# Performance work log

Measured on AMD Instinct MI355X. Metric: run time of the kernel, lower is better.

The kernel has to match this reference:

```python
import jax, jax.numpy as jnp
import numpy as np

T, B, V, E, HID, K = 1024, 128, 65536, 128, 256, 64
H = HID // 2  # per-direction LSTM hidden


def setup_inputs() -> dict:
    key = jax.random.key(0)
    ks = jax.random.split(key, 18)
    s = 0.05
    f32 = jnp.float32
    return {
        "kmers": jax.random.randint(ks[0], (T, B), 0, V),
        "tags": jax.random.randint(ks[1], (B,), 0, K),
        "emb": jax.random.normal(ks[2], (V, E), f32) * s,
        "w_ih_f": jax.random.normal(ks[3], (4 * H, E), f32) * s,
        "w_hh_f": jax.random.normal(ks[4], (4 * H, H), f32) * s,
        "b_ih_f": jax.random.normal(ks[5], (4 * H,), f32) * s,
        "b_hh_f": jax.random.normal(ks[6], (4 * H,), f32) * s,
        "w_ih_b": jax.random.normal(ks[7], (4 * H, E), f32) * s,
        "w_hh_b": jax.random.normal(ks[8], (4 * H, H), f32) * s,
        "b_ih_b": jax.random.normal(ks[9], (4 * H,), f32) * s,
        "b_hh_b": jax.random.normal(ks[10], (4 * H,), f32) * s,
        "w_proj": jax.random.normal(ks[11], (K, HID), f32) * s,
        "b_proj": jax.random.normal(ks[12], (K,), f32) * s,
        "start_trans": jax.random.uniform(ks[13], (K,), f32, -0.1, 0.1),
        "end_trans": jax.random.uniform(ks[14], (K,), f32, -0.1, 0.1),
        "trans": jax.random.uniform(ks[15], (K, K), f32, -0.1, 0.1),
    }


def _lstm_dir(x, w_ih, w_hh, b_ih, b_hh):
    # x: [T, B, E] -> hidden states [T, B, H]; PyTorch gate order i,f,g,o
    b = b_ih + b_hh
    xg = jnp.einsum('tbe,ge->tbg', x, w_ih) + b  # precompute input gates
    Bd = x.shape[1]
    Hd = w_hh.shape[1]
    def step(carry, g_in):
        h, c = carry
        g = g_in + h @ w_hh.T
        i, f, gg, o = jnp.split(g, 4, axis=-1)
        c = jax.nn.sigmoid(f) * c + jax.nn.sigmoid(i) * jnp.tanh(gg)
        h = jax.nn.sigmoid(o) * jnp.tanh(c)
        return (h, c), h
    init = (jnp.zeros((Bd, Hd), x.dtype), jnp.zeros((Bd, Hd), x.dtype))
    _, hs = jax.lax.scan(step, init, xg)
    return hs


def reference(kmers, tags, emb, w_ih_f, w_hh_f, b_ih_f, b_hh_f,
              w_ih_b, w_hh_b, b_ih_b, b_hh_b, w_proj, b_proj,
              start_trans, end_trans, trans):
    x = emb[kmers]  # [T, B, E]
    h_f = _lstm_dir(x, w_ih_f, w_hh_f, b_ih_f, b_hh_f)
    h_b = _lstm_dir(x[::-1], w_ih_b, w_hh_b, b_ih_b, b_hh_b)[::-1]
    out = jnp.concatenate([h_f, h_b], axis=-1)  # [T, B, HID]
    emissions = jnp.einsum('tbh,kh->tbk', out, w_proj) + b_proj  # [T, B, K]

    # tags repeated along time (original: tags.repeat(sent_size, 1))
    tags_seq = jnp.broadcast_to(tags[None, :], (emissions.shape[0], tags.shape[0]))

    # CRF numerator: score of given tag sequence (full mask)
    em_sel = jnp.take_along_axis(emissions, tags_seq[:, :, None], axis=2)[..., 0]  # [T, B]
    numerator = (start_trans[tags_seq[0]] + em_sel.sum(0)
                 + trans[tags_seq[:-1], tags_seq[1:]].sum(0)
                 + end_trans[tags_seq[-1]])  # [B]

    # CRF denominator: forward algorithm (log partition)
    def fwd_step(score, em_t):
        # score: [B, K] -> logsumexp over previous tag
        nxt = jax.nn.logsumexp(score[:, :, None] + trans[None, :, :] + em_t[:, None, :], axis=1)
        return nxt, None
    init = start_trans[None, :] + emissions[0]  # [B, K]
    final, _ = jax.lax.scan(fwd_step, init, emissions[1:])
    denominator = jax.nn.logsumexp(final + end_trans[None, :], axis=1)  # [B]

    # torchcrf default reduction='sum'; module returns negated llh
    return (denominator - numerator).sum()
```

## Files before the change

### kernel.cpp

```cpp
#include <hip/hip_runtime.h>
#include <hip/hip_bf16.h>

typedef _Float16 half8_t __attribute__((ext_vector_type(8)));
typedef _Float16 half4_t __attribute__((ext_vector_type(4)));
typedef _Float16 half2_t __attribute__((ext_vector_type(2)));
typedef float float4_t __attribute__((ext_vector_type(4)));
typedef unsigned int uint2_t __attribute__((ext_vector_type(2)));

#define TT 1024
#define BB 128
#define EE 128
#define HH 128
#define NTAG 64
#define ASTR 144

__device__ __forceinline__ float fast_exp(float x) {
  return __builtin_amdgcn_exp2f(x * 1.44269504088896f);
}
__device__ __forceinline__ void lds_barrier() {
  asm volatile("s_waitcnt lgkmcnt(0)\n\ts_barrier" ::: "memory");
}
__device__ __forceinline__ void lds_fence() {
  asm volatile("s_waitcnt lgkmcnt(0)" ::: "memory");
}
__device__ __forceinline__ half2_t cvt_pk(float a, float b) {
  return __builtin_bit_cast(half2_t, __builtin_amdgcn_cvt_pkrtz(a, b));
}
__device__ __forceinline__ half2_t h2bc(float v) {
  _Float16 h = (_Float16)v;
  half2_t r; r[0] = h; r[1] = h;
  return r;
}
__device__ __forceinline__ half8_t h8bc(float v) {
  _Float16 h = (_Float16)v;
  half8_t r;
#pragma unroll
  for (int i = 0; i < 8; ++i) r[i] = h;
  return r;
}
__device__ __forceinline__ float quad_max4(float v) {
  unsigned a = __builtin_bit_cast(unsigned, v);
  uint2_t r = __builtin_amdgcn_permlane32_swap(a, a, false, false);
  float m = fmaxf(__builtin_bit_cast(float, r[0]), __builtin_bit_cast(float, r[1]));
  unsigned b = __builtin_bit_cast(unsigned, m);
  uint2_t s = __builtin_amdgcn_permlane16_swap(b, b, false, false);
  return fmaxf(__builtin_bit_cast(float, s[0]), __builtin_bit_cast(float, s[1]));
}
__device__ __forceinline__ half2_t tanh6(half2_t x) {
  half2_t y = __builtin_elementwise_min(__builtin_elementwise_max(x, h2bc(-1.6f)), h2bc(1.6f));
  half2_t u = y * y;
  half2_t p = u * h2bc(0.04667f) + h2bc(-0.28507f);
  p = u * p + h2bc(1.0f);
  return y * p;
}
__device__ __forceinline__ half2_t sig6(half2_t x) {
  half2_t y = __builtin_elementwise_min(__builtin_elementwise_max(x, h2bc(-3.2f)), h2bc(3.2f));
  half2_t u = y * y;
  half2_t q = u * h2bc(0.00072921875f) + h2bc(-0.017816875f);
  q = u * q + h2bc(0.25f);
  return y * q + h2bc(0.5f);
}

__global__ __launch_bounds__(256) void initembed_kernel(const int* __restrict__ kmers,
                                                        const float* __restrict__ emb,
                                                        half4_t* __restrict__ x,
                                                        float4_t* __restrict__ state,
                                                        float* __restrict__ out) {
  if (blockIdx.x < 48) {
    if (blockIdx.x == 0 && threadIdx.x == 0) out[0] = 0.f;
    state[blockIdx.x * 256 + threadIdx.x] = (float4_t){0.f, 0.f, 0.f, 0.f};
    return;
  }
  const int g = (blockIdx.x - 48) * 256 + threadIdx.x;
  const int row = g >> 5, seg = g & 31;
  const int km = kmers[row];
  const float4_t v = ((const float4_t*)(emb + (size_t)km * EE))[seg];
  half4_t o;
  o[0] = (_Float16)v[0]; o[1] = (_Float16)v[1];
  o[2] = (_Float16)v[2]; o[3] = (_Float16)v[3];
  x[(size_t)row * 32 + seg] = o;
}

__device__ __forceinline__ void xg_body(
    int wg, int tid, const _Float16* __restrict__ x,
    const float* __restrict__ w_ih_f, const float* __restrict__ b_ih_f, const float* __restrict__ b_hh_f,
    const float* __restrict__ w_ih_b, const float* __restrict__ b_ih_b, const float* __restrict__ b_hh_b,
    _Float16* __restrict__ xgbuf, int s, int Tseg) {
  const int nt = Tseg >> 4;
  const int dir = wg / (8 * nt);
  const int rem = wg - dir * 8 * nt;
  const int chunk = rem / nt;
  const int tb = rem - chunk * nt;
  const int wave = tid >> 6, lane = tid & 63;
  const int n16 = lane & 15, quad = lane >> 4;

  const float* wih = dir ? w_ih_b : w_ih_f;
  const float* bih = dir ? b_ih_b : b_ih_f;
  const float* bhh = dir ? b_hh_b : b_hh_f;

  half8_t wf[4][4];
#pragma unroll
  for (int g = 0; g < 4; ++g) {
    const int row = g * HH + wave * 16 + n16;
#pragma unroll
    for (int kf = 0; kf < 4; ++kf) {
      const float* src = wih + row * EE + kf * 32 + quad * 8;
#pragma unroll
      for (int i = 0; i < 8; ++i) wf[g][kf][i] = (_Float16)src[i];
    }
  }
  float4_t bias4[4];
#pragma unroll
  for (int g = 0; g < 4; ++g) {
    const int row = g * HH + wave * 16 + quad * 4;
    const float4_t bi = *(const float4_t*)(bih + row);
    const float4_t bh = *(const float4_t*)(bhh + row);
    bias4[g] = bi + bh;
  }

  const int l0 = tb * 16;
  half8_t xb[4];
  {
    const int te = dir ? (TT - 1 - (s * Tseg + l0)) : (s * Tseg + l0);
#pragma unroll
    for (int kf = 0; kf < 4; ++kf)
      xb[kf] = *(const half8_t*)(x + ((size_t)te * BB + chunk * 16 + n16) * EE + kf * 32 + quad * 8);
  }
  for (int u = 0; u < 16; ++u) {
    const int l = l0 + u;
    half8_t xn[4] = {};
    if (u < 15) {
      const int tn = dir ? (TT - 1 - (s * Tseg + l + 1)) : (s * Tseg + l + 1);
#pragma unroll
      for (int kf = 0; kf < 4; ++kf)
        xn[kf] = *(const half8_t*)(x + ((size_t)tn * BB + chunk * 16 + n16) * EE + kf * 32 + quad * 8);
    }
    float4_t acc[4];
#pragma unroll
    for (int g = 0; g < 4; ++g) acc[g] = bias4[g];
#pragma unroll
    for (int kf = 0; kf < 4; ++kf)
#pragma unroll
      for (int g = 0; g < 4; ++g)
        acc[g] = __builtin_amdgcn_mfma_f32_16x16x32_f16(wf[g][kf], xb[kf], acc[g], 0, 0, 0);
    half8_t ho0, ho1;
#pragma unroll
    for (int r = 0; r < 4; ++r) {
      ho0[r] = (_Float16)acc[0][r];
      ho0[4 + r] = (_Float16)acc[1][r];
      ho1[r] = (_Float16)acc[2][r];
      ho1[4 + r] = (_Float16)acc[3][r];
    }
    _Float16* ob = xgbuf + (size_t)dir * Tseg * 65536 + (size_t)l * 65536 + chunk * 8192 +
                   wave * 1024 + lane * 16;
    *(half8_t*)ob = ho0;
    *(half8_t*)(ob + 8) = ho1;
#pragma unroll
    for (int kf = 0; kf < 4; ++kf) xb[kf] = xn[kf];
  }
}

__global__ __launch_bounds__(512) void xg_kernel(
    const _Float16* __restrict__ x,
    const float* __restrict__ w_ih_f, const float* __restrict__ b_ih_f, const float* __restrict__ b_hh_f,
    const float* __restrict__ w_ih_b, const float* __restrict__ b_ih_b, const float* __restrict__ b_hh_b,
    _Float16* __restrict__ xgbuf, int s, int Tseg) {
  xg_body(blockIdx.x, threadIdx.x, x, w_ih_f, b_ih_f, b_hh_f, w_ih_b, b_ih_b, b_hh_b, xgbuf, s,
          Tseg);
}

__global__ __launch_bounds__(512, 2) void lstm_xg_kernel(
    const _Float16* __restrict__ xgrd, _Float16* __restrict__ xgwr,
    const _Float16* __restrict__ x,
    const float* __restrict__ w_hh_f, const float* __restrict__ w_hh_b,
    const float* __restrict__ w_ih_f, const float* __restrict__ b_ih_f, const float* __restrict__ b_hh_f,
    const float* __restrict__ w_ih_b, const float* __restrict__ b_ih_b, const float* __restrict__ b_hh_b,
    _Float16* __restrict__ h_cat, _Float16* __restrict__ h_state, float* __restrict__ c_state,
    int s, int sx, int Tseg) {
  __shared__ _Float16 A[2][16 * ASTR];
  if (blockIdx.x >= 16) {
    xg_body(blockIdx.x - 16, threadIdx.x, x, w_ih_f, b_ih_f, b_hh_f, w_ih_b, b_ih_b, b_hh_b,
            xgwr, sx, Tseg);
    return;
  }
  const int wg = blockIdx.x;
  const int dir = wg >> 3, chunk = wg & 7;
  const int b0 = chunk * 16;
  const float* w_hh = dir ? w_hh_b : w_hh_f;
  const int tid = threadIdx.x;
  const int wave = tid >> 6, lane = tid & 63;
  const int n16 = lane & 15, quad = lane >> 4;

  half8_t wf[4][4];
#pragma unroll
  for (int g = 0; g < 4; ++g) {
    const int row = g * HH + wave * 16 + n16;
#pragma unroll
    for (int kf = 0; kf < 4; ++kf) {
      const float* src = w_hh + row * HH + kf * 32 + quad * 8;
#pragma unroll
      for (int i = 0; i < 8; ++i) wf[g][kf][i] = (_Float16)src[i];
    }
  }
  const int sidx = ((wg * 8 + wave) * 64 + lane) * 4;
  half4_t h4 = *(const half4_t*)(h_state + sidx);
  float4_t c4 = *(const float4_t*)(c_state + sidx);
  half2_t c2[2];
  c2[0] = cvt_pk(c4[0], c4[1]);
  c2[1] = cvt_pk(c4[2], c4[3]);
  *(half4_t*)(&A[0][n16 * ASTR + wave * 16 + quad * 4]) = h4;

  const _Float16* xgw =
      xgrd + (size_t)dir * Tseg * 65536 + chunk * 8192 + wave * 1024 + (size_t)lane * 16;
  half4_t hlast = h4;
  const float4_t z4 = {0.f, 0.f, 0.f, 0.f};
  const int te0 = dir ? (TT - 1 - s * Tseg) : (s * Tseg);
  _Float16* gp_run =
      h_cat + ((size_t)te0 * BB + b0 + n16) * 256 + dir * HH + wave * 16 + quad * 4;
  const ptrdiff_t dstep = dir ? -(ptrdiff_t)32768 : (ptrdiff_t)32768;

  half8_t pf0[4], pf1[4];
#pragma unroll
  for (int j = 0; j < 4; ++j) {
    const _Float16* p = xgw + (size_t)j * 65536;
    pf0[j] = *(const half8_t*)p;
    pf1[j] = *(const half8_t*)(p + 8);
  }

#define LSTM_STEP(AB, AN, X0, X1)                                                          \
  {                                                                                        \
    const _Float16* Abp = &AB[0];                                                          \
    _Float16* Anp = &AN[0];                                                                \
    half8_t hb0 = *(const half8_t*)(Abp + n16 * ASTR + 0 * 32 + quad * 8);                 \
    half8_t hb1 = *(const half8_t*)(Abp + n16 * ASTR + 1 * 32 + quad * 8);                 \
    half8_t hb2 = *(const half8_t*)(Abp + n16 * ASTR + 2 * 32 + quad * 8);                 \
    half8_t hb3 = *(const half8_t*)(Abp + n16 * ASTR + 3 * 32 + quad * 8);                 \
    float4_t acc[4];                                                                       \
    _Pragma("unroll") for (int g = 0; g < 4; ++g) {                                        \
      acc[g] = __builtin_amdgcn_mfma_f32_16x16x32_f16(wf[g][0], hb0, z4, 0, 0, 0);         \
    }                                                                                      \
    _Pragma("unroll") for (int g = 0; g < 4; ++g) {                                        \
      acc[g] = __builtin_amdgcn_mfma_f32_16x16x32_f16(wf[g][1], hb1, acc[g], 0, 0, 0);     \
    }                                                                                      \
    _Pragma("unroll") for (int g = 0; g < 4; ++g) {                                        \
      acc[g] = __builtin_amdgcn_mfma_f32_16x16x32_f16(wf[g][2], hb2, acc[g], 0, 0, 0);     \
    }                                                                                      \
    _Pragma("unroll") for (int g = 0; g < 4; ++g) {                                        \
      acc[g] = __builtin_amdgcn_mfma_f32_16x16x32_f16(wf[g][3], hb3, acc[g], 0, 0, 0);     \
    }                                                                                      \
    const half2_t* x0p = (const half2_t*)&X0;                                              \
    const half2_t* x1p = (const half2_t*)&X1;                                              \
    half4_t hstore;                                                                        \
    _Pragma("unroll") for (int p = 0; p < 2; ++p) {                                        \
      const half2_t i_ = sig6(cvt_pk(acc[0][2 * p], acc[0][2 * p + 1]) + x0p[p]);          \
      const half2_t f_ = sig6(cvt_pk(acc[1][2 * p], acc[1][2 * p + 1]) + x0p[2 + p]);      \
      const half2_t g_ = tanh6(cvt_pk(acc[2][2 * p], acc[2][2 * p + 1]) + x1p[p]);         \
      const half2_t o_ = sig6(cvt_pk(acc[3][2 * p], acc[3][2 * p + 1]) + x1p[2 + p]);      \
      c2[p] = f_ * c2[p] + i_ * g_;                                                        \
      const half2_t hh = o_ * tanh6(c2[p]);                                                \
      hstore[2 * p] = hh[0];                                                               \
      hstore[2 * p + 1] = hh[1];                                                           \
    }                                                                                      \
    *(half4_t*)(Anp + n16 * ASTR + wave * 16 + quad * 4) = hstore;                         \
    *(half4_t*)gp_run = hstore;                                                            \
    hlast = hstore;                                                                        \
  }

  for (int il = 0; il < Tseg - 4; il += 4) {
#pragma unroll
    for (int j = 0; j < 4; ++j) {
      lds_barrier();
      if (j & 1) {
        LSTM_STEP(A[1], A[0], pf0[j], pf1[j]);
      } else {
        LSTM_STEP(A[0], A[1], pf0[j], pf1[j]);
      }
      const _Float16* p = xgw + (size_t)(il + j + 4) * 65536;
      pf0[j] = *(const half8_t*)p;
      pf1[j] = *(const half8_t*)(p + 8);
      gp_run += dstep;
    }
  }
#pragma unroll
  for (int j = 0; j < 4; ++j) {
    lds_barrier();
    if (j & 1) {
      LSTM_STEP(A[1], A[0], pf0[j], pf1[j]);
    } else {
      LSTM_STEP(A[0], A[1], pf0[j], pf1[j]);
    }
    gp_run += dstep;
  }
#undef LSTM_STEP

  *(half4_t*)(h_state + sidx) = hlast;
  c4[0] = (float)c2[0][0]; c4[1] = (float)c2[0][1];
  c4[2] = (float)c2[1][0]; c4[3] = (float)c2[1][1];
  *(float4_t*)(c_state + sidx) = c4;
}

__global__ __launch_bounds__(256) void emis_kernel(const _Float16* __restrict__ h_cat,
                                                   const float* __restrict__ w_proj,
                                                   const float* __restrict__ b_proj,
                                                   float* __restrict__ em,
                                                   _Float16* __restrict__ expem) {
  const int tid = threadIdx.x;
  const int wave = tid >> 6, lane = tid & 63;
  const int n16 = lane & 15, quad = lane >> 4;
  const size_t row0 = (size_t)blockIdx.x * 64 + wave * 16;

  half8_t bf[4][8];
#pragma unroll
  for (int nt = 0; nt < 4; ++nt) {
    const float* wp = w_proj + (nt * 16 + n16) * 256;
#pragma unroll
    for (int kf = 0; kf < 8; ++kf) {
      const int kb = kf * 32 + quad * 8;
#pragma unroll
      for (int i = 0; i < 8; ++i) bf[nt][kf][i] = (_Float16)wp[kb + i];
    }
  }
  float4_t acc[4];
#pragma unroll
  for (int nt = 0; nt < 4; ++nt) {
    const float bv = b_proj[nt * 16 + n16];
    acc[nt] = (float4_t){bv, bv, bv, bv};
  }
#pragma unroll
  for (int kf = 0; kf < 8; ++kf) {
    half8_t af = *(const half8_t*)(h_cat + (row0 + n16) * 256 + kf * 32 + quad * 8);
#pragma unroll
    for (int nt = 0; nt < 4; ++nt)
      acc[nt] = __builtin_amdgcn_mfma_f32_16x16x32_f16(af, bf[nt][kf], acc[nt], 0, 0, 0);
  }
#pragma unroll
  for (int nt = 0; nt < 4; ++nt)
#pragma unroll
    for (int r = 0; r < 4; ++r) {
      const size_t idx = (row0 + quad * 4 + r) * NTAG + nt * 16 + n16;
      em[idx] = acc[nt][r];
      expem[idx] = (_Float16)fast_exp(acc[nt][r]);
    }
}

__global__ __launch_bounds__(64) void mcrf_kernel(const float* __restrict__ em,
                                                  const _Float16* __restrict__ expem,
                                                  const float* __restrict__ trans,
                                                  const int* __restrict__ tags,
                                                  const float* __restrict__ start_trans,
                                                  const float* __restrict__ end_trans,
                                                  _Float16* __restrict__ Nbuf,
                                                  float* __restrict__ lzbuf,
                                                  float* __restrict__ num) {
  const int lane = threadIdx.x;
  if (blockIdx.x >= 2048) {
    const int nb = blockIdx.x - 2048;
    const int tg = tags[nb];
    float acc = 0.f;
    for (int t = lane; t < TT; t += 64)
      acc += em[((size_t)t * BB + nb) * NTAG + tg];
#pragma unroll
    for (int off = 32; off > 0; off >>= 1) acc += __shfl_xor(acc, off, 64);
    if (lane == 0)
      num[nb] = start_trans[tg] + end_trans[tg] + 1023.0f * trans[tg * NTAG + tg] + acc;
    return;
  }
  const int n16 = lane & 15, quad = lane >> 4;
  const int b = blockIdx.x >> 4;
  const int s = blockIdx.x & 15;

  half8_t efA[4][2];
#pragma unroll
  for (int mt = 0; mt < 4; ++mt)
#pragma unroll
    for (int kf = 0; kf < 2; ++kf)
#pragma unroll
      for (int i = 0; i < 8; ++i) {
        const int m = mt * 16 + n16, k = kf * 32 + quad * 8 + i;
        efA[mt][kf][i] = (_Float16)(fast_exp(trans[k * NTAG + m]) * 0.015625f);
      }

  half8_t pb[4][2];
#pragma unroll
  for (int tile = 0; tile < 4; ++tile)
#pragma unroll
    for (int kf = 0; kf < 2; ++kf)
#pragma unroll
      for (int i = 0; i < 8; ++i) {
        const int k = kf * 32 + quad * 8 + i;
        pb[tile][kf][i] = (_Float16)((k == tile * 16 + n16) ? 1.f : 0.f);
      }

  float lz2 = 0.f;
  const float4_t z4 = {0.f, 0.f, 0.f, 0.f};
  const _Float16* exb = expem + (size_t)b * NTAG;
  const int t0 = s * 64 + 1;
  const int nsteps = (s == 15) ? 63 : 64;

#define MCRF_CORE(PB0, PB1, NB0, NB1)                                                      \
  {                                                                                        \
    float4_t a0 = __builtin_amdgcn_mfma_f32_16x16x32_f16(efA[0][0], PB0, z4, 0, 0, 0);     \
    float4_t a1 = __builtin_amdgcn_mfma_f32_16x16x32_f16(efA[1][0], PB0, z4, 0, 0, 0);     \
    float4_t a2 = __builtin_amdgcn_mfma_f32_16x16x32_f16(efA[2][0], PB0, z4, 0, 0, 0);     \
    float4_t a3 = __builtin_amdgcn_mfma_f32_16x16x32_f16(efA[3][0], PB0, z4, 0, 0, 0);     \
    a0 = __builtin_amdgcn_mfma_f32_16x16x32_f16(efA[0][1], PB1, a0, 0, 0, 0);              \
    a1 = __builtin_amdgcn_mfma_f32_16x16x32_f16(efA[1][1], PB1, a1, 0, 0, 0);              \
    a2 = __builtin_amdgcn_mfma_f32_16x16x32_f16(efA[2][1], PB1, a2, 0, 0, 0);              \
    a3 = __builtin_amdgcn_mfma_f32_16x16x32_f16(efA[3][1], PB1, a3, 0, 0, 0);              \
    half2_t dpk[4][2];                                                                     \
    dpk[0][0] = cvt_pk(a0[0], a0[1]); dpk[0][1] = cvt_pk(a0[2], a0[3]);                    \
    dpk[1][0] = cvt_pk(a1[0], a1[1]); dpk[1][1] = cvt_pk(a1[2], a1[3]);                    \
    dpk[2][0] = cvt_pk(a2[0], a2[1]); dpk[2][1] = cvt_pk(a2[2], a2[3]);                    \
    dpk[3][0] = cvt_pk(a3[0], a3[1]); dpk[3][1] = cvt_pk(a3[2], a3[3]);                    \
    half2_t* wwp0 = (half2_t*)&NB0;                                                        \
    half2_t* wwp1 = (half2_t*)&NB1;                                                        \
    _Pragma("unroll") for (int kf = 0; kf < 2; ++kf) {                                     \
      half2_t* wp = kf ? wwp1 : wwp0;                                                      \
      _Pragma("unroll") for (int p = 0; p < 2; ++p) {                                      \
        const unsigned Xu = __builtin_bit_cast(unsigned, dpk[2 * kf][p]);                  \
        const unsigned Yu = __builtin_bit_cast(unsigned, dpk[2 * kf + 1][p]);              \
        uint2_t r1 = __builtin_amdgcn_permlane32_swap(Xu, Yu, false, false);               \
        uint2_t r2 = __builtin_amdgcn_permlane16_swap(r1[0], r1[1], false, false);         \
        wp[p] = __builtin_bit_cast(half2_t, r2[0]);                                        \
        wp[2 + p] = __builtin_bit_cast(half2_t, r2[1]);                                    \
      }                                                                                    \
    }                                                                                      \
  }

#define MSTEP(GC0, GC1, IT)                                                                \
  {                                                                                        \
    _Pragma("unroll") for (int tile = 0; tile < 4; ++tile) {                               \
      half8_t nb0, nb1;                                                                    \
      MCRF_CORE(pb[tile][0], pb[tile][1], nb0, nb1)                                        \
      pb[tile][0] = nb0 * GC0;                                                             \
      pb[tile][1] = nb1 * GC1;                                                             \
    }                                                                                      \
    if (((IT) & 15) == 15) {                                                               \
      half8_t m8 = __builtin_elementwise_max(pb[0][0], pb[0][1]);                          \
      m8 = __builtin_elementwise_max(m8, __builtin_elementwise_max(pb[1][0], pb[1][1]));   \
      m8 = __builtin_elementwise_max(m8, __builtin_elementwise_max(pb[2][0], pb[2][1]));   \
      m8 = __builtin_elementwise_max(m8, __builtin_elementwise_max(pb[3][0], pb[3][1]));   \
      float mm = (float)m8[0];                                                             \
      _Pragma("unroll") for (int i = 1; i < 8; ++i) mm = fmaxf(mm, (float)m8[i]);          \
      mm = quad_max4(mm);                                                                  \
      mm = fmaxf(mm, __shfl_xor(mm, 1, 64));                                               \
      mm = fmaxf(mm, __shfl_xor(mm, 2, 64));                                               \
      mm = fmaxf(mm, __shfl_xor(mm, 4, 64));                                               \
      mm = fmaxf(mm, __shfl_xor(mm, 8, 64));                                               \
      lz2 += __builtin_amdgcn_logf(mm);                                                    \
      const half8_t rc8 = h8bc(__builtin_amdgcn_rcpf(mm));                                 \
      _Pragma("unroll") for (int tile = 0; tile < 4; ++tile) {                             \
        pb[tile][0] *= rc8;                                                                \
        pb[tile][1] *= rc8;                                                                \
      }                                                                                    \
    }                                                                                      \
  }

  half8_t pre0[4], pre1[4];
#pragma unroll
  for (int j = 0; j < 4; ++j) {
    const size_t tt = (size_t)(t0 + j) * 8192;
    pre0[j] = *(const half8_t*)(exb + tt + quad * 8);
    pre1[j] = *(const half8_t*)(exb + tt + 32 + quad * 8);
  }
  int it = 0;
  const int full4 = nsteps >> 2;
  for (int grp = 0; grp < full4; ++grp) {
#pragma unroll
    for (int j = 0; j < 4; ++j) {
      const half8_t gc0 = pre0[j], gc1 = pre1[j];
      int tf = t0 + it + 4;
      tf = tf > 1023 ? 1023 : tf;
      const size_t tt = (size_t)tf * 8192;
      pre0[j] = *(const half8_t*)(exb + tt + quad * 8);
      pre1[j] = *(const half8_t*)(exb + tt + 32 + quad * 8);
      MSTEP(gc0, gc1, it)
      ++it;
    }
  }
  for (; it < nsteps; ++it) {
    const size_t tt = (size_t)(t0 + it) * 8192;
    const half8_t gc0 = *(const half8_t*)(exb + tt + quad * 8);
    const half8_t gc1 = *(const half8_t*)(exb + tt + 32 + quad * 8);
    MSTEP(gc0, gc1, it)
  }
#undef MSTEP
#undef MCRF_CORE

  _Float16* nb = Nbuf + ((size_t)b * 16 + s) * 4096;
#pragma unroll
  for (int tile = 0; tile < 4; ++tile) {
    const int col = tile * 16 + n16;
#pragma unroll
    for (int kf = 0; kf < 2; ++kf)
      *(half8_t*)(nb + (size_t)col * 64 + kf * 32 + quad * 8) = pb[tile][kf];
  }
  if (lane == 0) lzbuf[b * 16 + s] = lz2;
}

__global__ __launch_bounds__(64) void merge_kernel(const _Float16* __restrict__ Nbuf,
                                                   const float* __restrict__ lzbuf,
                                                   const float* __restrict__ em,
                                                   const float* __restrict__ start_trans,
                                                   const float* __restrict__ end_trans,
                                                   const float* __restrict__ num,
                                                   float* __restrict__ out) {
  const int b = blockIdx.x, m = threadIdx.x;
  __shared__ float w[64];
  float L2 = 0.f;
  w[m] = fast_exp(end_trans[m]);
  for (int s = 15; s >= 0; --s) {
    lds_fence();
    const _Float16* row = Nbuf + (((size_t)b * 16 + s) * 64 + m) * 64;
    float acc = 0.f;
#pragma unroll
    for (int kf = 0; kf < 8; ++kf) {
      const half8_t rv = *(const half8_t*)(row + kf * 8);
#pragma unroll
      for (int i = 0; i < 8; ++i) acc += (float)rv[i] * w[kf * 8 + i];
    }
    float mx = acc;
#pragma unroll
    for (int off = 32; off > 0; off >>= 1) mx = fmaxf(mx, __shfl_xor(mx, off, 64));
    L2 += __builtin_amdgcn_logf(mx) + lzbuf[b * 16 + s];
    const float inv = __builtin_amdgcn_rcpf(mx);
    lds_fence();
    w[m] = acc * inv;
  }
  lds_fence();
  const float sv = start_trans[m] + em[(size_t)b * NTAG + m];
  float m0 = sv;
#pragma unroll
  for (int off = 32; off > 0; off >>= 1) m0 = fmaxf(m0, __shfl_xor(m0, off, 64));
  float z = fast_exp(sv - m0) * w[m];
#pragma unroll
  for (int off = 32; off > 0; off >>= 1) z += __shfl_xor(z, off, 64);
  if (m == 0) {
    const float denomv =
        m0 + 0.693147180559945f * (L2 + 6138.0f + __builtin_amdgcn_logf(z));
    atomicAdd(out, denomv - num[b]);
  }
}

extern "C" void kernel_launch(void* const* d_in, const int* in_sizes, int n_in,
                              void* d_out, int out_size, void* d_ws, size_t ws_size,
                              hipStream_t stream) {
  const int* kmers = (const int*)d_in[0];
  const int* tags = (const int*)d_in[1];
  const float* emb = (const float*)d_in[2];
  const float* w_ih_f = (const float*)d_in[3];
  const float* w_hh_f = (const float*)d_in[4];
  const float* b_ih_f = (const float*)d_in[5];
  const float* b_hh_f = (const float*)d_in[6];
  const float* w_ih_b = (const float*)d_in[7];
  const float* w_hh_b = (const float*)d_in[8];
  const float* b_ih_b = (const float*)d_in[9];
  const float* b_hh_b = (const float*)d_in[10];
  const float* w_proj = (const float*)d_in[11];
  const float* b_proj = (const float*)d_in[12];
  const float* start_trans = (const float*)d_in[13];
  const float* end_trans = (const float*)d_in[14];
  const float* trans = (const float*)d_in[15];

  char* ws = (char*)d_ws;
  half4_t* x = (half4_t*)ws;
  _Float16* h_cat = (_Float16*)(ws + 33554432);
  float* em = (float*)ws;
  float* out = (float*)d_out;
  _Float16* Nbuf = (_Float16*)(ws + 33554432);
  float* lzbuf = (float*)(ws + 33554432 + 16777216);
  float* num = (float*)(ws + 33554432 + 16785920);

  const bool fused = ws_size >= 235078656ull;
  if (fused) {
    const int Tseg = 256;
    _Float16* buf0 = (_Float16*)(ws + 100663296);
    _Float16* buf1 = (_Float16*)(ws + 100663296 + 67108864);
    _Float16* expem = (_Float16*)(ws + 100663296);
    _Float16* h_state = (_Float16*)(ws + 100663296 + 134217728);
    float* c_state = (float*)(ws + 100663296 + 134217728 + 65536);

    hipLaunchKernelGGL(initembed_kernel, dim3(16432), dim3(256), 0, stream, kmers, emb, x,
                       (float4_t*)h_state, out);
    hipLaunchKernelGGL(xg_kernel, dim3(Tseg), dim3(512), 0, stream, (const _Float16*)x,
                       w_ih_f, b_ih_f, b_hh_f, w_ih_b, b_ih_b, b_hh_b, buf0, 0, Tseg);
    for (int s = 0; s < 3; ++s) {
      _Float16* rd = (s & 1) ? buf1 : buf0;
      _Float16* wr = (s & 1) ? buf0 : buf1;
      hipLaunchKernelGGL(lstm_xg_kernel, dim3(16 + Tseg), dim3(512), 0, stream,
                         (const _Float16*)rd, wr, (const _Float16*)x, w_hh_f, w_hh_b,
                         w_ih_f, b_ih_f, b_hh_f, w_ih_b, b_ih_b, b_hh_b,
                         h_cat, h_state, c_state, s, s + 1, Tseg);
    }
    hipLaunchKernelGGL(lstm_xg_kernel, dim3(16), dim3(512), 0, stream,
                       (const _Float16*)buf1, buf0, (const _Float16*)x, w_hh_f, w_hh_b,
                       w_ih_f, b_ih_f, b_hh_f, w_ih_b, b_ih_b, b_hh_b,
                       h_cat, h_state, c_state, 3, 0, Tseg);
    hipLaunchKernelGGL(emis_kernel, dim3(2048), dim3(256), 0, stream, h_cat, w_proj, b_proj, em,
                       expem);
    hipLaunchKernelGGL(mcrf_kernel, dim3(2176), dim3(64), 0, stream, em,
                       (const _Float16*)expem, trans, tags, start_trans, end_trans, Nbuf, lzbuf,
                       num);
    hipLaunchKernelGGL(merge_kernel, dim3(128), dim3(64), 0, stream, (const _Float16*)Nbuf,
                       lzbuf, em, start_trans, end_trans, num, out);
  } else {
    int nseg;
    if (ws_size >= 167969792ull) nseg = 4;
    else if (ws_size >= 134415360ull) nseg = 8;
    else nseg = 16;
    const int Tseg = TT / nseg;
    const size_t xg_bytes = 268435456ull / (size_t)nseg;
    _Float16* xgbuf = (_Float16*)(ws + 100663296);
    _Float16* expem = (_Float16*)(ws + 100663296);
    _Float16* h_state = (_Float16*)(ws + 100663296 + xg_bytes);
    float* c_state = (float*)(ws + 100663296 + xg_bytes + 65536);

    hipLaunchKernelGGL(initembed_kernel, dim3(16432), dim3(256), 0, stream, kmers, emb, x,
                       (float4_t*)h_state, out);
    for (int s = 0; s < nseg; ++s) {
      hipLaunchKernelGGL(xg_kernel, dim3(Tseg), dim3(512), 0, stream, (const _Float16*)x,
                         w_ih_f, b_ih_f, b_hh_f, w_ih_b, b_ih_b, b_hh_b, xgbuf, s, Tseg);
      hipLaunchKernelGGL(lstm_xg_kernel, dim3(16), dim3(512), 0, stream,
                         (const _Float16*)xgbuf, xgbuf, (const _Float16*)x, w_hh_f, w_hh_b,
                         w_ih_f, b_ih_f, b_hh_f, w_ih_b, b_ih_b, b_hh_b,
                         h_cat, h_state, c_state, s, s, Tseg);
    }
    hipLaunchKernelGGL(emis_kernel, dim3(2048), dim3(256), 0, stream, h_cat, w_proj, b_proj, em,
                       expem);
    hipLaunchKernelGGL(mcrf_kernel, dim3(2176), dim3(64), 0, stream, em,
                       (const _Float16*)expem, trans, tags, start_trans, end_trans, Nbuf, lzbuf,
                       num);
    hipLaunchKernelGGL(merge_kernel, dim3(128), dim3(64), 0, stream, (const _Float16*)Nbuf,
                       lzbuf, em, start_trans, end_trans, num, out);
  }
}
```

Baseline: 957.8 us.

## Fuse embedding gather into xg GEMM and overlap emissions with last LSTM segment

Drops the separate embedding-gather kernel and the fp16 x buffer. The xg GEMM now reads kmers and converts emb rows to fp16 on the fly, and the state zeroing moves into extra blocks of the first xg launch. In the fused path, the final LSTM segment launch adds 512 blocks that compute emissions for timesteps already finished in earlier segments, so the leftover emis_kernel only handles the rest. This cuts a launch and a write/read pass over x and overlaps projection work with the serial recurrence, at the cost of redundant emb gathers and w_proj fp32 loads in the inner loop.

```diff
diff --git a/kernel.cpp b/kernel.cpp
--- a/kernel.cpp
+++ b/kernel.cpp
@@ -60,29 +60,19 @@
   q = u * q + h2bc(0.25f);
   return y * q + h2bc(0.5f);
 }
-
-__global__ __launch_bounds__(256) void initembed_kernel(const int* __restrict__ kmers,
-                                                        const float* __restrict__ emb,
-                                                        half4_t* __restrict__ x,
-                                                        float4_t* __restrict__ state,
-                                                        float* __restrict__ out) {
-  if (blockIdx.x < 48) {
-    if (blockIdx.x == 0 && threadIdx.x == 0) out[0] = 0.f;
-    state[blockIdx.x * 256 + threadIdx.x] = (float4_t){0.f, 0.f, 0.f, 0.f};
-    return;
-  }
-  const int g = (blockIdx.x - 48) * 256 + threadIdx.x;
-  const int row = g >> 5, seg = g & 31;
-  const int km = kmers[row];
-  const float4_t v = ((const float4_t*)(emb + (size_t)km * EE))[seg];
-  half4_t o;
-  o[0] = (_Float16)v[0]; o[1] = (_Float16)v[1];
-  o[2] = (_Float16)v[2]; o[3] = (_Float16)v[3];
-  x[(size_t)row * 32 + seg] = o;
+__device__ __forceinline__ half8_t emb8(const float* __restrict__ p) {
+  const float4_t lo = *(const float4_t*)p;
+  const float4_t hi = *(const float4_t*)(p + 4);
+  half8_t v;
+  v[0] = (_Float16)lo[0]; v[1] = (_Float16)lo[1];
+  v[2] = (_Float16)lo[2]; v[3] = (_Float16)lo[3];
+  v[4] = (_Float16)hi[0]; v[5] = (_Float16)hi[1];
+  v[6] = (_Float16)hi[2]; v[7] = (_Float16)hi[3];
+  return v;
 }
 
 __device__ __forceinline__ void xg_body(
-    int wg, int tid, const _Float16* __restrict__ x,
+    int wg, int tid, const int* __restrict__ kmers, const float* __restrict__ emb,
     const float* __restrict__ w_ih_f, const float* __restrict__ b_ih_f, const float* __restrict__ b_hh_f,
     const float* __restrict__ w_ih_b, const float* __restrict__ b_ih_b, const float* __restrict__ b_hh_b,
     _Float16* __restrict__ xgbuf, int s, int Tseg) {
@@ -118,22 +108,25 @@
     bias4[g] = bi + bh;
   }
 
+  const int bidx = chunk * 16 + n16;
   const int l0 = tb * 16;
   half8_t xb[4];
   {
     const int te = dir ? (TT - 1 - (s * Tseg + l0)) : (s * Tseg + l0);
-#pragma unroll
-    for (int kf = 0; kf < 4; ++kf)
-      xb[kf] = *(const half8_t*)(x + ((size_t)te * BB + chunk * 16 + n16) * EE + kf * 32 + quad * 8);
+    const int km = kmers[te * BB + bidx];
+    const float* er = emb + (size_t)km * EE;
+#pragma unroll
+    for (int kf = 0; kf < 4; ++kf) xb[kf] = emb8(er + kf * 32 + quad * 8);
   }
   for (int u = 0; u < 16; ++u) {
     const int l = l0 + u;
     half8_t xn[4] = {};
     if (u < 15) {
       const int tn = dir ? (TT - 1 - (s * Tseg + l + 1)) : (s * Tseg + l + 1);
-#pragma unroll
-      for (int kf = 0; kf < 4; ++kf)
-        xn[kf] = *(const half8_t*)(x + ((size_t)tn * BB + chunk * 16 + n16) * EE + kf * 32 + quad * 8);
+      const int kmn = kmers[tn * BB + bidx];
+      const float* er = emb + (size_t)kmn * EE;
+#pragma unroll
+      for (int kf = 0; kf < 4; ++kf) xn[kf] = emb8(er + kf * 32 + quad * 8);
     }
     float4_t acc[4];
 #pragma unroll
@@ -160,27 +153,79 @@
   }
 }
 
+__device__ __forceinline__ void emis_unit(int u, int tid, const _Float16* __restrict__ h_cat,
+                                          const float* __restrict__ w_proj,
+                                          const float* __restrict__ b_proj,
+                                          float* __restrict__ em,
+                                          _Float16* __restrict__ expem) {
+  const int wave = tid >> 6, lane = tid & 63;
+  const int n16 = lane & 15, quad = lane >> 4;
+  const size_t row0 = (size_t)u * 64 + wave * 16;
+
+  float4_t acc[4];
+#pragma unroll
+  for (int nt = 0; nt < 4; ++nt) {
+    const float bv = b_proj[nt * 16 + n16];
+    acc[nt] = (float4_t){bv, bv, bv, bv};
+  }
+#pragma unroll
+  for (int kf = 0; kf < 8; ++kf) {
+    const half8_t af = *(const half8_t*)(h_cat + (row0 + n16) * 256 + kf * 32 + quad * 8);
+    const int kb = kf * 32 + quad * 8;
+#pragma unroll
+    for (int nt = 0; nt < 4; ++nt) {
+      const float* wp = w_proj + (nt * 16 + n16) * 256 + kb;
+      half8_t bf;
+#pragma unroll
+      for (int i = 0; i < 8; ++i) bf[i] = (_Float16)wp[i];
+      acc[nt] = __builtin_amdgcn_mfma_f32_16x16x32_f16(af, bf, acc[nt], 0, 0, 0);
+    }
+  }
+#pragma unroll
+  for (int nt = 0; nt < 4; ++nt)
+#pragma unroll
+    for (int r = 0; r < 4; ++r) {
+      const size_t idx = (row0 + quad * 4 + r) * NTAG + nt * 16 + n16;
+      em[idx] = acc[nt][r];
+      expem[idx] = (_Float16)fast_exp(acc[nt][r]);
+    }
+}
+
 __global__ __launch_bounds__(512) void xg_kernel(
-    const _Float16* __restrict__ x,
+    const int* __restrict__ kmers, const float* __restrict__ emb,
     const float* __restrict__ w_ih_f, const float* __restrict__ b_ih_f, const float* __restrict__ b_hh_f,
     const float* __restrict__ w_ih_b, const float* __restrict__ b_ih_b, const float* __restrict__ b_hh_b,
-    _Float16* __restrict__ xgbuf, int s, int Tseg) {
-  xg_body(blockIdx.x, threadIdx.x, x, w_ih_f, b_ih_f, b_hh_f, w_ih_b, b_ih_b, b_hh_b, xgbuf, s,
-          Tseg);
+    _Float16* __restrict__ xgbuf, int s, int Tseg,
+    float4_t* __restrict__ zstate, float* __restrict__ out) {
+  if (blockIdx.x >= (unsigned)Tseg) {
+    const int zb = blockIdx.x - Tseg;
+    if (threadIdx.x < 256) zstate[zb * 256 + threadIdx.x] = (float4_t){0.f, 0.f, 0.f, 0.f};
+    if (zb == 0 && threadIdx.x == 511) out[0] = 0.f;
+    return;
+  }
+  xg_body(blockIdx.x, threadIdx.x, kmers, emb, w_ih_f, b_ih_f, b_hh_f, w_ih_b, b_ih_b, b_hh_b,
+          xgbuf, s, Tseg);
 }
 
 __global__ __launch_bounds__(512, 2) void lstm_xg_kernel(
     const _Float16* __restrict__ xgrd, _Float16* __restrict__ xgwr,
-    const _Float16* __restrict__ x,
+    const int* __restrict__ kmers, const float* __restrict__ emb,
     const float* __restrict__ w_hh_f, const float* __restrict__ w_hh_b,
     const float* __restrict__ w_ih_f, const float* __restrict__ b_ih_f, const float* __restrict__ b_hh_f,
     const float* __restrict__ w_ih_b, const float* __restrict__ b_ih_b, const float* __restrict__ b_hh_b,
     _Float16* __restrict__ h_cat, _Float16* __restrict__ h_state, float* __restrict__ c_state,
+    const float* __restrict__ w_proj, const float* __restrict__ b_proj,
+    float* __restrict__ em, _Float16* __restrict__ expem,
     int s, int sx, int Tseg) {
   __shared__ _Float16 A[2][16 * ASTR];
   if (blockIdx.x >= 16) {
-    xg_body(blockIdx.x - 16, threadIdx.x, x, w_ih_f, b_ih_f, b_hh_f, w_ih_b, b_ih_b, b_hh_b,
-            xgwr, sx, Tseg);
+    if (sx >= 0) {
+      xg_body(blockIdx.x - 16, threadIdx.x, kmers, emb, w_ih_f, b_ih_f, b_hh_f, w_ih_b, b_ih_b,
+              b_hh_b, xgwr, sx, Tseg);
+    } else {
+      const int u = 512 + (blockIdx.x - 16) * 2 + (threadIdx.x >> 8);
+      emis_unit(u, threadIdx.x & 255, h_cat, w_proj, b_proj, em, expem);
+    }
     return;
   }
   const int wg = blockIdx.x;
@@ -299,48 +344,14 @@
   *(float4_t*)(c_state + sidx) = c4;
 }
 
-__global__ __launch_bounds__(256) void emis_kernel(const _Float16* __restrict__ h_cat,
+__global__ __launch_bounds__(512) void emis_kernel(const _Float16* __restrict__ h_cat,
                                                    const float* __restrict__ w_proj,
                                                    const float* __restrict__ b_proj,
                                                    float* __restrict__ em,
-                                                   _Float16* __restrict__ expem) {
-  const int tid = threadIdx.x;
-  const int wave = tid >> 6, lane = tid & 63;
-  const int n16 = lane & 15, quad = lane >> 4;
-  const size_t row0 = (size_t)blockIdx.x * 64 + wave * 16;
-
-  half8_t bf[4][8];
-#pragma unroll
-  for (int nt = 0; nt < 4; ++nt) {
-    const float* wp = w_proj + (nt * 16 + n16) * 256;
-#pragma unroll
-    for (int kf = 0; kf < 8; ++kf) {
-      const int kb = kf * 32 + quad * 8;
-#pragma unroll
-      for (int i = 0; i < 8; ++i) bf[nt][kf][i] = (_Float16)wp[kb + i];
-    }
-  }
-  float4_t acc[4];
-#pragma unroll
-  for (int nt = 0; nt < 4; ++nt) {
-    const float bv = b_proj[nt * 16 + n16];
-    acc[nt] = (float4_t){bv, bv, bv, bv};
-  }
-#pragma unroll
-  for (int kf = 0; kf < 8; ++kf) {
-    half8_t af = *(const half8_t*)(h_cat + (row0 + n16) * 256 + kf * 32 + quad * 8);
-#pragma unroll
-    for (int nt = 0; nt < 4; ++nt)
-      acc[nt] = __builtin_amdgcn_mfma_f32_16x16x32_f16(af, bf[nt][kf], acc[nt], 0, 0, 0);
-  }
-#pragma unroll
-  for (int nt = 0; nt < 4; ++nt)
-#pragma unroll
-    for (int r = 0; r < 4; ++r) {
-      const size_t idx = (row0 + quad * 4 + r) * NTAG + nt * 16 + n16;
-      em[idx] = acc[nt][r];
-      expem[idx] = (_Float16)fast_exp(acc[nt][r]);
-    }
+                                                   _Float16* __restrict__ expem, int mode) {
+  int u = blockIdx.x * 2 + (threadIdx.x >> 8);
+  if (mode) u = (u < 512) ? u : u + 1024;
+  emis_unit(u, threadIdx.x & 255, h_cat, w_proj, b_proj, em, expem);
 }
 
 __global__ __launch_bounds__(64) void mcrf_kernel(const float* __restrict__ em,
@@ -563,7 +574,6 @@
   const float* trans = (const float*)d_in[15];
 
   char* ws = (char*)d_ws;
-  half4_t* x = (half4_t*)ws;
   _Float16* h_cat = (_Float16*)(ws + 33554432);
   float* em = (float*)ws;
   float* out = (float*)d_out;
@@ -580,24 +590,23 @@
     _Float16* h_state = (_Float16*)(ws + 100663296 + 134217728);
     float* c_state = (float*)(ws + 100663296 + 134217728 + 65536);
 
-    hipLaunchKernelGGL(initembed_kernel, dim3(16432), dim3(256), 0, stream, kmers, emb, x,
+    hipLaunchKernelGGL(xg_kernel, dim3(Tseg + 49), dim3(512), 0, stream, kmers, emb,
+                       w_ih_f, b_ih_f, b_hh_f, w_ih_b, b_ih_b, b_hh_b, buf0, 0, Tseg,
                        (float4_t*)h_state, out);
-    hipLaunchKernelGGL(xg_kernel, dim3(Tseg), dim3(512), 0, stream, (const _Float16*)x,
-                       w_ih_f, b_ih_f, b_hh_f, w_ih_b, b_ih_b, b_hh_b, buf0, 0, Tseg);
     for (int s = 0; s < 3; ++s) {
       _Float16* rd = (s & 1) ? buf1 : buf0;
       _Float16* wr = (s & 1) ? buf0 : buf1;
       hipLaunchKernelGGL(lstm_xg_kernel, dim3(16 + Tseg), dim3(512), 0, stream,
-                         (const _Float16*)rd, wr, (const _Float16*)x, w_hh_f, w_hh_b,
+                         (const _Float16*)rd, wr, kmers, emb, w_hh_f, w_hh_b,
                          w_ih_f, b_ih_f, b_hh_f, w_ih_b, b_ih_b, b_hh_b,
-                         h_cat, h_state, c_state, s, s + 1, Tseg);
-    }
-    hipLaunchKernelGGL(lstm_xg_kernel, dim3(16), dim3(512), 0, stream,
-                       (const _Float16*)buf1, buf0, (const _Float16*)x, w_hh_f, w_hh_b,
+                         h_cat, h_state, c_state, w_proj, b_proj, em, expem, s, s + 1, Tseg);
+    }
+    hipLaunchKernelGGL(lstm_xg_kernel, dim3(16 + 512), dim3(512), 0, stream,
+                       (const _Float16*)buf1, buf0, kmers, emb, w_hh_f, w_hh_b,
                        w_ih_f, b_ih_f, b_hh_f, w_ih_b, b_ih_b, b_hh_b,
-                       h_cat, h_state, c_state, 3, 0, Tseg);
-    hipLaunchKernelGGL(emis_kernel, dim3(2048), dim3(256), 0, stream, h_cat, w_proj, b_proj, em,
-                       expem);
+                       h_cat, h_state, c_state, w_proj, b_proj, em, expem, 3, -1, Tseg);
+    hipLaunchKernelGGL(emis_kernel, dim3(512), dim3(512), 0, stream, h_cat, w_proj, b_proj, em,
+                       expem, 1);
     hipLaunchKernelGGL(mcrf_kernel, dim3(2176), dim3(64), 0, stream, em,
                        (const _Float16*)expem, trans, tags, start_trans, end_trans, Nbuf, lzbuf,
                        num);
@@ -615,18 +624,18 @@
     _Float16* h_state = (_Float16*)(ws + 100663296 + xg_bytes);
     float* c_state = (float*)(ws + 100663296 + xg_bytes + 65536);
 
-    hipLaunchKernelGGL(initembed_kernel, dim3(16432), dim3(256), 0, stream, kmers, emb, x,
-                       (float4_t*)h_state, out);
     for (int s = 0; s < nseg; ++s) {
-      hipLaunchKernelGGL(xg_kernel, dim3(Tseg), dim3(512), 0, stream, (const _Float16*)x,
-                         w_ih_f, b_ih_f, b_hh_f, w_ih_b, b_ih_b, b_hh_b, xgbuf, s, Tseg);
+      const int extra = (s == 0) ? 49 : 0;
+      hipLaunchKernelGGL(xg_kernel, dim3(Tseg + extra), dim3(512), 0, stream, kmers, emb,
+                         w_ih_f, b_ih_f, b_hh_f, w_ih_b, b_ih_b, b_hh_b, xgbuf, s, Tseg,
+                         (float4_t*)h_state, out);
       hipLaunchKernelGGL(lstm_xg_kernel, dim3(16), dim3(512), 0, stream,
-                         (const _Float16*)xgbuf, xgbuf, (const _Float16*)x, w_hh_f, w_hh_b,
+                         (const _Float16*)xgbuf, xgbuf, kmers, emb, w_hh_f, w_hh_b,
                          w_ih_f, b_ih_f, b_hh_f, w_ih_b, b_ih_b, b_hh_b,
-                         h_cat, h_state, c_state, s, s, Tseg);
-    }
-    hipLaunchKernelGGL(emis_kernel, dim3(2048), dim3(256), 0, stream, h_cat, w_proj, b_proj, em,
-                       expem);
+                         h_cat, h_state, c_state, w_proj, b_proj, em, expem, s, 0, Tseg);
+    }
+    hipLaunchKernelGGL(emis_kernel, dim3(1024), dim3(512), 0, stream, h_cat, w_proj, b_proj, em,
+                       expem, 0);
     hipLaunchKernelGGL(mcrf_kernel, dim3(2176), dim3(64), 0, stream, em,
                        (const _Float16*)expem, trans, tags, start_trans, end_trans, Nbuf, lzbuf,
                        num);
```

Result: faster. 930.1 us (-2.9%).
